# Optimization experiments

Measured on AMD Instinct MI355X. Metric: run time of the kernel, lower is better.

## Reference

```python
import jax, jax.numpy as jnp
import numpy as np

B, C, L = 8, 512, 8192
H = 8  # head_count
DK = C // H  # head key channels
DV = C // H  # head value channels


def setup_inputs() -> dict:
    key = jax.random.key(0)
    ks = jax.random.split(key, 10)
    s = 1.0 / np.sqrt(C)
    return {
        "input_": jax.random.normal(ks[0], (B, C, L), jnp.float32),
        "context_": jax.random.normal(ks[1], (B, C, L), jnp.float32),
        "Wk": jax.random.normal(ks[2], (C, C), jnp.float32) * s,
        "bk": jax.random.normal(ks[3], (C,), jnp.float32) * 0.01,
        "Wq": jax.random.normal(ks[4], (C, C), jnp.float32) * s,
        "bq": jax.random.normal(ks[5], (C,), jnp.float32) * 0.01,
        "Wv": jax.random.normal(ks[6], (C, C), jnp.float32) * s,
        "bv": jax.random.normal(ks[7], (C,), jnp.float32) * 0.01,
        "Wr": jax.random.normal(ks[8], (C, C), jnp.float32) * s,
        "br": jax.random.normal(ks[9], (C,), jnp.float32) * 0.01,
    }


def _proj(W, b, x):
    # 1x1 Conv1d == channel matmul: [O,C] x [B,C,L] -> [B,O,L]
    return jnp.einsum('oc,bcl->bol', W, x) + b[None, :, None]


def reference(input_, context_, Wk, bk, Wq, bq, Wv, bv, Wr, br):
    b, _, l = input_.shape
    keys = _proj(Wk, bk, context_).reshape(b, H, DK, l)
    queries = _proj(Wq, bq, input_).reshape(b, H, DK, l)
    values = _proj(Wv, bv, context_).reshape(b, H, DV, l)
    # per-head: softmax(K) over sequence, softmax(Q) over head-key channels
    k = jax.nn.softmax(keys, axis=3)
    q = jax.nn.softmax(queries, axis=2)
    # context = K @ V^T : [b,h,dk,dv]
    ctx = jnp.einsum('bhkl,bhvl->bhkv', k, values)
    # attended = context^T @ Q : [b,h,dv,l]
    att = jnp.einsum('bhkv,bhkl->bhvl', ctx, q).reshape(b, H * DV, l)
    return _proj(Wr, br, att) + input_
```

## Files before the change

kernel.cpp:

```cpp
#include <hip/hip_runtime.h>

#define NB 8
#define NC 512
#define NL 8192
#define NH 8
#define ND 64

typedef float f32x4 __attribute__((ext_vector_type(4)));
typedef __bf16 bf16x8 __attribute__((ext_vector_type(8)));
typedef unsigned int u32x4 __attribute__((ext_vector_type(4)));

__device__ __forceinline__ unsigned short f2bf(float f) {
    unsigned u = __builtin_bit_cast(unsigned, f);
    u += 0x7fffu + ((u >> 16) & 1u);
    return (unsigned short)(u >> 16);
}
__device__ __forceinline__ bf16x8 frag_from_u32x4(u32x4 v) {
    return __builtin_bit_cast(bf16x8, v);
}
__device__ __forceinline__ bf16x8 ld_frag_lds(const unsigned short* p) {
    const unsigned* q = (const unsigned*)p;
    u32x4 v = { q[0], q[1], q[2], q[3] };
    return frag_from_u32x4(v);
}
__device__ __forceinline__ bf16x8 ld_frag_g16(const unsigned short* p) {
    return frag_from_u32x4(*(const u32x4*)p);
}
__device__ __forceinline__ bf16x8 ldL(const unsigned short* Lb, unsigned off) {
    return frag_from_u32x4(*(const u32x4*)((const char*)Lb + off));
}

__device__ __forceinline__ void gload16(const unsigned short* g, unsigned short* l) {
    __builtin_amdgcn_global_load_lds(
        (const __attribute__((address_space(1))) unsigned int*)g,
        (__attribute__((address_space(3))) unsigned int*)l, 16, 0, 0);
}

__device__ __forceinline__ void prep_body(int i,
    const float* __restrict__ Wk, const float* __restrict__ Wv,
    const float* __restrict__ Wq, const float* __restrict__ Wr,
    const float* __restrict__ bk, const float* __restrict__ bv,
    unsigned short* __restrict__ Wb, float* __restrict__ bkv, float* __restrict__ zf)
{
    const int WN = NC * NC;
    if (i < 4 * WN) {
        const float* src = (i < WN) ? Wk : (i < 2 * WN) ? Wv : (i < 3 * WN) ? Wq : Wr;
        Wb[i] = f2bf(src[i & (WN - 1)]);
    } else if (i < 4 * WN + 2 * NC) {
        int j = i - 4 * WN;
        bkv[j] = (j < NC) ? bk[j] : bv[j - NC];
    } else {
        zf[i - (4 * WN + 2 * NC)] = 0.f;
    }
}

__device__ __forceinline__ int ltidx(int c, int l) {
    return c * 64 + ((((l) >> 2) ^ ((c >> 2) & 15)) << 2) + (l & 3);
}
__global__ __launch_bounds__(256) void transpose_prep_kernel(
    const float* __restrict__ X0, const float* __restrict__ X1,
    unsigned short* __restrict__ Y0, unsigned short* __restrict__ Y1,
    const float* __restrict__ Wk, const float* __restrict__ Wv,
    const float* __restrict__ Wq, const float* __restrict__ Wr,
    const float* __restrict__ bk, const float* __restrict__ bv,
    unsigned short* __restrict__ Wb, float* __restrict__ bkv, float* __restrict__ zf)
{
    const int bz = blockIdx.z;
    const int t = threadIdx.x;
    if (bz == 2 * NB) {
        constexpr int total = 4 * NC * NC + 2 * NC + (NB * NH * ND * ND + NB * NC);
        const int stride = (NL / 64) * (NC / 64) * 256;
        for (int i = (blockIdx.y * (NL / 64) + blockIdx.x) * 256 + t; i < total; i += stride)
            prep_body(i, Wk, Wv, Wq, Wr, bk, bv, Wb, bkv, zf);
        return;
    }
    const float* X = (bz < NB) ? X0 : X1;
    unsigned short* Y = (bz < NB) ? Y0 : Y1;
    const int b = bz & (NB - 1);
    const int l0 = blockIdx.x * 64, c0 = blockIdx.y * 64;
    __shared__ alignas(16) unsigned short lt[64 * 64];
    const float* Xb = X + (size_t)b * NC * NL;
    #pragma unroll
    for (int it = 0; it < 4; ++it) {
        const int c = it * 16 + (t >> 4), l4 = (t & 15) * 4;
        f32x4 v = *(const f32x4*)(Xb + (size_t)(c0 + c) * NL + l0 + l4);
        unsigned lo = f2bf(v.x) | ((unsigned)f2bf(v.y) << 16);
        unsigned hi = f2bf(v.z) | ((unsigned)f2bf(v.w) << 16);
        unsigned* p = (unsigned*)&lt[ltidx(c, l4)];
        p[0] = lo; p[1] = hi;
    }
    __syncthreads();
    unsigned short* Yb = Y + (size_t)b * NL * NC;
    #pragma unroll
    for (int it = 0; it < 2; ++it) {
        const int l = it * 32 + (t >> 3), c8 = (t & 7) * 8;
        u32x4 o;
        #pragma unroll
        for (int d = 0; d < 4; ++d) {
            unsigned lo = lt[ltidx(c8 + 2 * d, l)];
            unsigned hi = lt[ltidx(c8 + 2 * d + 1, l)];
            o[d] = lo | (hi << 16);
        }
        *(u32x4*)(Yb + (size_t)(l0 + l) * NC + c0 + c8) = o;
    }
}

__device__ __forceinline__ void stage_half(
    unsigned short* __restrict__ Ld, const unsigned short* __restrict__ Gs,
    int t, int wave)
{
    #pragma unroll
    for (int c = 0; c < 2; ++c) {
        const int idx = c * 512 + t;
        const int r = idx >> 3;
        const int ch = (idx & 7) ^ (r & 7);
        gload16(Gs + (size_t)r * NC + ch * 8, Ld + (size_t)(c * 512 + wave * 64) * 8);
    }
}

template<int MT, bool RESID, bool PERB, bool EXPK>
__global__ __launch_bounds__(512) void gemm8_kernel(
    const unsigned short* __restrict__ Wb,
    const unsigned short* __restrict__ Xt,
    const float* __restrict__ bias,
    const float* __restrict__ resid,
    void* __restrict__ Yv)
{
    const int bx = blockIdx.x;
    const int g  = bx >> 3;
    const int mt = g % MT;
    const int nt = (g / MT) * 8 + (bx & 7);
    const int b  = blockIdx.y;
    const int t  = threadIdx.x;
    const int wave = t >> 6, lane = t & 63;
    const int m0 = mt * 256, n0 = nt * 256;
    const int wm = wave >> 2, wn = wave & 3;
    const int OC = MT * 256;

    __shared__ alignas(16) unsigned short L[65536];

    f32x4 acc[8][4] = {};

    const unsigned short* Wp = Wb + (PERB ? (size_t)b * NC * NC : 0) + (size_t)m0 * NC;
    const unsigned short* Xp = Xt + (size_t)b * NL * NC + (size_t)n0 * NC;

    const int lr = lane & 15, qg = lane >> 4;
    const unsigned xr = (unsigned)(lr & 7);
    const unsigned cq0 = (((unsigned)qg) ^ xr) * 16u;
    const unsigned cq1 = (((unsigned)qg + 4u) ^ xr) * 16u;
    const unsigned aB = (unsigned)(wm * 16384 + lr * 128);
    const unsigned bB = 32768u + (unsigned)((wn >> 1) * 16384 + ((wn & 1) * 64 + lr) * 128);

    #define STA(par, half, kt) stage_half(&L[(par) * 32768 + (half) * 8192], \
        Wp + (size_t)((half) * 128) * NC + (kt) * 64, t, wave)
    #define STB(par, half, kt) stage_half(&L[(par) * 32768 + 16384 + (half) * 8192], \
        Xp + (size_t)((half) * 128) * NC + (kt) * 64, t, wave)

    STA(0, 0, 0); STA(0, 1, 0); STB(0, 0, 0); STB(0, 1, 0);
    STA(1, 0, 1); STA(1, 1, 1); STB(1, 0, 1); STB(1, 1, 1);
    __builtin_amdgcn_sched_barrier(0);
    asm volatile("s_waitcnt vmcnt(8)" ::: "memory");
    __builtin_amdgcn_sched_barrier(0);
    __builtin_amdgcn_s_barrier();
    __builtin_amdgcn_sched_barrier(0);

    for (int kt = 0; kt < 8; ++kt) {
        const unsigned parB = (unsigned)((kt & 1) * 65536);
        const int par = kt & 1, ks = kt + 2;
        bf16x8 bf[4][2];
        #pragma unroll
        for (int q4 = 0; q4 < 4; ++q4) {
            if (q4 == 0) {
                #pragma unroll
                for (int j = 0; j < 4; ++j) {
                    bf[j][0] = ldL(L, parB + bB + j * 2048 + cq0);
                    bf[j][1] = ldL(L, parB + bB + j * 2048 + cq1);
                }
            }
            bf16x8 af[2][2];
            #pragma unroll
            for (int di = 0; di < 2; ++di) {
                af[di][0] = ldL(L, parB + aB + (q4 * 2 + di) * 2048 + cq0);
                af[di][1] = ldL(L, parB + aB + (q4 * 2 + di) * 2048 + cq1);
            }
            if (ks < 8) {
                if (q4 == 1)      { STB(par, 0, ks); }
                else if (q4 == 2) { STB(par, 1, ks); }
                else if (q4 == 3) { STA(par, 0, ks); STA(par, 1, ks); }
            }
            __builtin_amdgcn_sched_barrier(0);
            __builtin_amdgcn_s_barrier();
            __builtin_amdgcn_sched_barrier(0);
            __builtin_amdgcn_s_setprio(1);
            #pragma unroll
            for (int di = 0; di < 2; ++di)
                #pragma unroll
                for (int j = 0; j < 4; ++j) {
                    acc[q4 * 2 + di][j] = __builtin_amdgcn_mfma_f32_16x16x32_bf16(
                        af[di][0], bf[j][0], acc[q4 * 2 + di][j], 0, 0, 0);
                    acc[q4 * 2 + di][j] = __builtin_amdgcn_mfma_f32_16x16x32_bf16(
                        af[di][1], bf[j][1], acc[q4 * 2 + di][j], 0, 0, 0);
                }
            __builtin_amdgcn_s_setprio(0);
            __builtin_amdgcn_sched_barrier(0);
            if (q4 == 3) {
                if (kt < 6)       asm volatile("s_waitcnt vmcnt(8)" ::: "memory");
                else if (kt == 6) asm volatile("s_waitcnt vmcnt(0)" ::: "memory");
                __builtin_amdgcn_sched_barrier(0);
            }
            __builtin_amdgcn_s_barrier();
            __builtin_amdgcn_sched_barrier(0);
        }
    }
    #undef STA
    #undef STB

    const int col = lr, row0 = qg * 4;
    if constexpr (EXPK) {
        unsigned short* Y = (unsigned short*)Yv;
        const bool isK = (m0 < NC);
        #pragma unroll
        for (int i = 0; i < 8; ++i)
            #pragma unroll
            for (int r = 0; r < 4; ++r) {
                const int o = m0 + wm * 128 + i * 16 + row0 + r;
                const float bo = bias[o];
                const size_t rb = (size_t)b * OC * NL + (size_t)o * NL + n0 + wn * 64;
                #pragma unroll
                for (int j = 0; j < 4; ++j) {
                    float v = acc[i][j][r] + bo;
                    if (isK) v = __expf(v);
                    Y[rb + j * 16 + col] = f2bf(v);
                }
            }
    } else if constexpr (RESID) {
        float* Y = (float*)Yv;
        #pragma unroll
        for (int i = 0; i < 8; ++i)
            #pragma unroll
            for (int r = 0; r < 4; ++r) {
                const int o = m0 + wm * 128 + i * 16 + row0 + r;
                const float bo = bias[o];
                const size_t rb = (size_t)b * OC * NL + (size_t)o * NL + n0 + wn * 64;
                #pragma unroll
                for (int j = 0; j < 4; ++j) {
                    const size_t idx = rb + j * 16 + col;
                    Y[idx] = acc[i][j][r] + bo + resid[idx];
                }
            }
    } else {
        unsigned short* Y = (unsigned short*)Yv;
        #pragma unroll
        for (int i = 0; i < 8; ++i)
            #pragma unroll
            for (int r = 0; r < 4; ++r) {
                const int o = m0 + wm * 128 + i * 16 + row0 + r;
                const float bo = bias[o];
                const size_t rb = (size_t)b * OC * NL + (size_t)o * NL + n0 + wn * 64;
                #pragma unroll
                for (int j = 0; j < 4; ++j)
                    Y[rb + j * 16 + col] = f2bf(acc[i][j][r] + bo);
            }
    }
}

template<int MT, bool RESID, bool PERB, bool QSMT, bool EXPK>
__global__ __launch_bounds__(256) void gemm_kernel(
    const unsigned short* __restrict__ Wb,
    const unsigned short* __restrict__ Xt,
    const float* __restrict__ bias,
    const float* __restrict__ resid,
    void* __restrict__ Yv)
{
    const int bx = blockIdx.x;
    const int g  = bx >> 3;
    const int mt = g % MT;
    const int nt = (g / MT) * 8 + (bx & 7);
    const int b  = blockIdx.y;
    const int t  = threadIdx.x;
    const int wave = t >> 6, lane = t & 63;
    const int m0 = mt * 128, n0 = nt * 128;
    const int wm = (wave & 1) * 64, wn = (wave >> 1) * 64;
    const int OC = MT * 128;

    __shared__ alignas(16) unsigned short lA[128 * 32];
    __shared__ alignas(16) unsigned short lX[128 * 32];

    f32x4 acc[4][4] = {};

    const unsigned short* Wp = Wb + (PERB ? (size_t)b * NC * NC : 0);
    const unsigned short* Xb = Xt + (size_t)b * NL * NC;

    const int lr = lane & 15, q = lane >> 4;
    const unsigned aoff = (unsigned)((wm + lr) * 64 + (q ^ (((wm + lr) >> 1) & 3)) * 16);
    const unsigned boff = (unsigned)((wn + lr) * 64 + (q ^ (((wn + lr) >> 1) & 3)) * 16);
    const int pb0 = wave * 128;

    for (int k0 = 0; k0 < NC; k0 += 32) {
        #pragma unroll
        for (int cc = 0; cc < 2; ++cc) {
            const int pb = pb0 + cc * 64;
            const int p  = pb + lane;
            const int r  = p >> 2;
            const int qq = (p & 3) ^ ((r >> 1) & 3);
            gload16(Wp + (size_t)(m0 + r) * NC + k0 + qq * 8, &lA[pb * 8]);
            gload16(Xb + (size_t)(n0 + r) * NC + k0 + qq * 8, &lX[pb * 8]);
        }
        __syncthreads();

        bf16x8 af[4], bfx[4];
        #pragma unroll
        for (int i = 0; i < 4; ++i)
            af[i] = frag_from_u32x4(*(const u32x4*)((const char*)lA + aoff + i * 1024));
        #pragma unroll
        for (int j = 0; j < 4; ++j)
            bfx[j] = frag_from_u32x4(*(const u32x4*)((const char*)lX + boff + j * 1024));
        #pragma unroll
        for (int i = 0; i < 4; ++i)
            #pragma unroll
            for (int j = 0; j < 4; ++j)
                acc[i][j] = __builtin_amdgcn_mfma_f32_16x16x32_bf16(af[i], bfx[j], acc[i][j], 0, 0, 0);
        __syncthreads();
    }

    const int col = lane & 15, row0 = (lane >> 4) * 4;

    if constexpr (QSMT) {
        #pragma unroll
        for (int i = 0; i < 4; ++i)
            #pragma unroll
            for (int r = 0; r < 4; ++r) {
                const float bo = bias[m0 + wm + i * 16 + row0 + r];
                #pragma unroll
                for (int j = 0; j < 4; ++j) acc[i][j][r] += bo;
            }
        float inv[4];
        #pragma unroll
        for (int j = 0; j < 4; ++j) {
            float m = -1e30f;
            #pragma unroll
            for (int i = 0; i < 4; ++i)
                #pragma unroll
                for (int r = 0; r < 4; ++r) m = fmaxf(m, acc[i][j][r]);
            m = fmaxf(m, __shfl_xor(m, 16));
            m = fmaxf(m, __shfl_xor(m, 32));
            float s = 0.f;
            #pragma unroll
            for (int i = 0; i < 4; ++i)
                #pragma unroll
                for (int r = 0; r < 4; ++r) {
                    const float e = __expf(acc[i][j][r] - m);
                    acc[i][j][r] = e;
                    s += e;
                }
            s += __shfl_xor(s, 16);
            s += __shfl_xor(s, 32);
            inv[j] = 1.0f / s;
        }
        unsigned short* Yq = (unsigned short*)Yv;
        #pragma unroll
        for (int j = 0; j < 4; ++j) {
            const size_t rowb = (size_t)b * NL * NC + (size_t)(n0 + wn + j * 16 + col) * NC;
            #pragma unroll
            for (int i = 0; i < 4; ++i) {
                const int o0 = m0 + wm + i * 16 + row0;
                unsigned lo = f2bf(acc[i][j][0] * inv[j]) | ((unsigned)f2bf(acc[i][j][1] * inv[j]) << 16);
                unsigned hi = f2bf(acc[i][j][2] * inv[j]) | ((unsigned)f2bf(acc[i][j][3] * inv[j]) << 16);
                *(unsigned long long*)(Yq + rowb + o0) =
                    (unsigned long long)lo | ((unsigned long long)hi << 32);
            }
        }
    } else if constexpr (EXPK) {
        unsigned short* Y = (unsigned short*)Yv;
        const bool isK = (m0 < NC);
        #pragma unroll
        for (int i = 0; i < 4; ++i)
            #pragma unroll
            for (int r = 0; r < 4; ++r) {
                const int o = m0 + wm + i * 16 + row0 + r;
                const float bo = bias[o];
                const size_t rb = (size_t)b * OC * NL + (size_t)o * NL + n0 + wn;
                #pragma unroll
                for (int j = 0; j < 4; ++j) {
                    float v = acc[i][j][r] + bo;
                    if (isK) v = __expf(v);
                    Y[rb + j * 16 + col] = f2bf(v);
                }
            }
    } else {
        #pragma unroll
        for (int i = 0; i < 4; ++i) {
            #pragma unroll
            for (int r = 0; r < 4; ++r) {
                const int o = m0 + wm + i * 16 + row0 + r;
                const float bo = bias[o];
                const size_t rb = (size_t)b * OC * NL + (size_t)o * NL + n0 + wn;
                if constexpr (RESID) {
                    float* Y = (float*)Yv;
                    #pragma unroll
                    for (int j = 0; j < 4; ++j) {
                        const size_t idx = rb + j * 16 + col;
                        Y[idx] = acc[i][j][r] + bo + resid[idx];
                    }
                } else {
                    unsigned short* Y = (unsigned short*)Yv;
                    #pragma unroll
                    for (int j = 0; j < 4; ++j)
                        Y[rb + j * 16 + col] = f2bf(acc[i][j][r] + bo);
                }
            }
        }
    }
}

__global__ __launch_bounds__(256) void ctx_kernel(
    const unsigned short* __restrict__ KV,
    float* __restrict__ ctx,
    float* __restrict__ rowsum)
{
    const int bh = blockIdx.x;
    const int sp = blockIdx.y;
    const int t = threadIdx.x;
    const int wave = t >> 6, lane = t & 63;
    const int b = bh >> 3, h = bh & 7;
    const size_t base_k = ((size_t)b * 2 * NC + h * ND) * NL;
    const size_t base_v = base_k + (size_t)NC * NL;
    const int i = wave * 16 + (lane & 15);
    const int koff = (lane >> 4) * 8;
    const unsigned short* Ka = KV + base_k + (size_t)i * NL + koff;

    const u32x4 onesw = { 0x3f803f80u, 0x3f803f80u, 0x3f803f80u, 0x3f803f80u };
    const bf16x8 onef = frag_from_u32x4(onesw);

    f32x4 acc[4] = {};
    f32x4 accs = {};
    const int l0 = sp * (NL / 16);
    for (int l = l0; l < l0 + (NL / 16); l += 32) {
        bf16x8 a = ld_frag_g16(Ka + l);
        #pragma unroll
        for (int j = 0; j < 4; ++j) {
            bf16x8 bv = ld_frag_g16(KV + base_v + (size_t)(j * 16 + (lane & 15)) * NL + l + koff);
            acc[j] = __builtin_amdgcn_mfma_f32_16x16x32_bf16(a, bv, acc[j], 0, 0, 0);
        }
        accs = __builtin_amdgcn_mfma_f32_16x16x32_bf16(a, onef, accs, 0, 0, 0);
    }
    const int col = lane & 15, row0 = (lane >> 4) * 4;
    #pragma unroll
    for (int j = 0; j < 4; ++j)
        #pragma unroll
        for (int r = 0; r < 4; ++r)
            atomicAdd(&ctx[(size_t)bh * (ND * ND) + (size_t)(wave * 16 + row0 + r) * ND + j * 16 + col],
                      acc[j][r]);
    if (col == 0) {
        #pragma unroll
        for (int r = 0; r < 4; ++r)
            atomicAdd(&rowsum[(size_t)b * NC + h * ND + wave * 16 + row0 + r], accs[r]);
    }
}

__global__ __launch_bounds__(512) void fold_kernel(
    const unsigned short* __restrict__ Wrb,
    const float* __restrict__ ctxb,
    const float* __restrict__ rowsum,
    unsigned short* __restrict__ Mb)
{
    const int bh = blockIdx.x;
    const int b = bh >> 3, h = bh & 7;
    const int t = threadIdx.x;
    const int wave = t >> 6, lane = t & 63;

    __shared__ unsigned short lc[64 * 66];
    const float* cs = ctxb + (size_t)bh * (ND * ND);
    const float* rs = rowsum + (size_t)b * NC + h * ND;
    #pragma unroll
    for (int it = 0; it < 8; ++it) {
        int i = it * 512 + t;
        lc[(i >> 6) * 66 + (i & 63)] = f2bf(cs[i] / rs[i >> 6]);
    }
    __syncthreads();

    const int koff = (lane >> 4) * 8;
    f32x4 acc[4][4] = {};
    #pragma unroll
    for (int kk = 0; kk < 64; kk += 32) {
        bf16x8 af[4], bfx[4];
        #pragma unroll
        for (int i = 0; i < 4; ++i)
            af[i] = ld_frag_g16(Wrb + (size_t)(wave * 64 + i * 16 + (lane & 15)) * NC
                                + h * ND + kk + koff);
        #pragma unroll
        for (int j = 0; j < 4; ++j)
            bfx[j] = ld_frag_lds(&lc[(j * 16 + (lane & 15)) * 66 + kk + koff]);
        #pragma unroll
        for (int i = 0; i < 4; ++i)
            #pragma unroll
            for (int j = 0; j < 4; ++j)
                acc[i][j] = __builtin_amdgcn_mfma_f32_16x16x32_bf16(af[i], bfx[j], acc[i][j], 0, 0, 0);
    }

    const int col = lane & 15, row0 = (lane >> 4) * 4;
    #pragma unroll
    for (int i = 0; i < 4; ++i)
        #pragma unroll
        for (int r = 0; r < 4; ++r) {
            const int o = wave * 64 + i * 16 + row0 + r;
            #pragma unroll
            for (int j = 0; j < 4; ++j)
                Mb[(size_t)b * NC * NC + (size_t)o * NC + h * ND + j * 16 + col]
                    = f2bf(acc[i][j][r]);
        }
}

extern "C" void kernel_launch(void* const* d_in, const int* in_sizes, int n_in,
                              void* d_out, int out_size, void* d_ws, size_t ws_size,
                              hipStream_t stream) {
    (void)in_sizes; (void)n_in; (void)out_size; (void)ws_size;
    const float* input_   = (const float*)d_in[0];
    const float* context_ = (const float*)d_in[1];
    const float* Wk = (const float*)d_in[2];
    const float* bk = (const float*)d_in[3];
    const float* Wq = (const float*)d_in[4];
    const float* bq = (const float*)d_in[5];
    const float* Wv = (const float*)d_in[6];
    const float* bv = (const float*)d_in[7];
    const float* Wr = (const float*)d_in[8];
    const float* br = (const float*)d_in[9];
    float* out = (float*)d_out;

    char* ws = (char*)d_ws;
    unsigned short* Wkvb = (unsigned short*)ws;
    unsigned short* Wqb  = Wkvb + 2 * NC * NC;
    unsigned short* Wrb  = Wqb + NC * NC;
    float* bkv  = (float*)(Wrb + NC * NC);
    float* ctxb = bkv + 2 * NC;
    float* rowsum = ctxb + NB * NH * ND * ND;
    unsigned short* KVp = (unsigned short*)(rowsum + NB * NC);
    unsigned short* R2  = KVp + (size_t)NB * 2 * NC * NL;
    unsigned short* Mb  = KVp;
    unsigned short* Xt_in = (unsigned short*)d_out;

    transpose_prep_kernel<<<dim3(NL / 64, NC / 64, 2 * NB + 1), 256, 0, stream>>>(
        context_, input_, R2, Xt_in,
        Wk, Wv, Wq, Wr, bk, bv, Wkvb, bkv, ctxb);

    gemm8_kernel<4, false, false, true><<<dim3(128, NB), 512, 0, stream>>>(
        Wkvb, R2, bkv, nullptr, KVp);

    gemm_kernel<4, false, false, true, false><<<dim3(256, NB), 256, 0, stream>>>(
        Wqb, Xt_in, bq, nullptr, R2);

    ctx_kernel<<<dim3(NB * NH, 16), 256, 0, stream>>>(KVp, ctxb, rowsum);
    fold_kernel<<<NB * NH, 512, 0, stream>>>(Wrb, ctxb, rowsum, Mb);

    gemm8_kernel<2, true, true, false><<<dim3(64, NB), 512, 0, stream>>>(
        Mb, R2, br, input_, out);
}
```

Measured before the change: 621.8 us.

## Move Q projection with softmax epilogue onto 256x256 gemm8 kernel; widen transpose tiles

Removes the older 128x128 gemm_kernel. The Q projection and its fused per-head channel softmax now run on the pipelined 512-thread gemm8 kernel with 256x256 tiles, where each wave covers two heads. This targets better data reuse and MFMA pipelining for the Q GEMM. The input transpose kernel also now handles 256 channels per block instead of 64, cutting the block count and using a larger LDS tile. In exchange, the grids are smaller, which risks lower occupancy and a heavier register load in the softmax epilogue.

```diff
diff --git a/kernel.cpp b/kernel.cpp
--- a/kernel.cpp
+++ b/kernel.cpp
@@ -69,7 +69,7 @@
     const int t = threadIdx.x;
     if (bz == 2 * NB) {
         constexpr int total = 4 * NC * NC + 2 * NC + (NB * NH * ND * ND + NB * NC);
-        const int stride = (NL / 64) * (NC / 64) * 256;
+        const int stride = (NL / 64) * (NC / 256) * 256;
         for (int i = (blockIdx.y * (NL / 64) + blockIdx.x) * 256 + t; i < total; i += stride)
             prep_body(i, Wk, Wv, Wq, Wr, bk, bv, Wb, bkv, zf);
         return;
@@ -77,11 +77,11 @@
     const float* X = (bz < NB) ? X0 : X1;
     unsigned short* Y = (bz < NB) ? Y0 : Y1;
     const int b = bz & (NB - 1);
-    const int l0 = blockIdx.x * 64, c0 = blockIdx.y * 64;
-    __shared__ alignas(16) unsigned short lt[64 * 64];
+    const int l0 = blockIdx.x * 64, c0 = blockIdx.y * 256;
+    __shared__ alignas(16) unsigned short lt[256 * 64];
     const float* Xb = X + (size_t)b * NC * NL;
     #pragma unroll
-    for (int it = 0; it < 4; ++it) {
+    for (int it = 0; it < 16; ++it) {
         const int c = it * 16 + (t >> 4), l4 = (t & 15) * 4;
         f32x4 v = *(const f32x4*)(Xb + (size_t)(c0 + c) * NL + l0 + l4);
         unsigned lo = f2bf(v.x) | ((unsigned)f2bf(v.y) << 16);
@@ -92,8 +92,8 @@
     __syncthreads();
     unsigned short* Yb = Y + (size_t)b * NL * NC;
     #pragma unroll
-    for (int it = 0; it < 2; ++it) {
-        const int l = it * 32 + (t >> 3), c8 = (t & 7) * 8;
+    for (int it = 0; it < 8; ++it) {
+        const int l = it * 8 + (t >> 5), c8 = (t & 31) * 8;
         u32x4 o;
         #pragma unroll
         for (int d = 0; d < 4; ++d) {
@@ -118,7 +118,7 @@
     }
 }
 
-template<int MT, bool RESID, bool PERB, bool EXPK>
+template<int MT, bool RESID, bool PERB, bool EXPK, bool QSMT>
 __global__ __launch_bounds__(512) void gemm8_kernel(
     const unsigned short* __restrict__ Wb,
     const unsigned short* __restrict__ Xt,
@@ -216,7 +216,55 @@
     #undef STB
 
     const int col = lr, row0 = qg * 4;
-    if constexpr (EXPK) {
+    if constexpr (QSMT) {
+        #pragma unroll
+        for (int i = 0; i < 8; ++i)
+            #pragma unroll
+            for (int r = 0; r < 4; ++r) {
+                const float bo = bias[m0 + wm * 128 + i * 16 + row0 + r];
+                #pragma unroll
+                for (int j = 0; j < 4; ++j) acc[i][j][r] += bo;
+            }
+        float inv[2][4];
+        #pragma unroll
+        for (int hh = 0; hh < 2; ++hh)
+            #pragma unroll
+            for (int j = 0; j < 4; ++j) {
+                float m = -1e30f;
+                #pragma unroll
+                for (int i = 0; i < 4; ++i)
+                    #pragma unroll
+                    for (int r = 0; r < 4; ++r) m = fmaxf(m, acc[hh * 4 + i][j][r]);
+                m = fmaxf(m, __shfl_xor(m, 16));
+                m = fmaxf(m, __shfl_xor(m, 32));
+                float s = 0.f;
+                #pragma unroll
+                for (int i = 0; i < 4; ++i)
+                    #pragma unroll
+                    for (int r = 0; r < 4; ++r) {
+                        const float e = __expf(acc[hh * 4 + i][j][r] - m);
+                        acc[hh * 4 + i][j][r] = e;
+                        s += e;
+                    }
+                s += __shfl_xor(s, 16);
+                s += __shfl_xor(s, 32);
+                inv[hh][j] = 1.0f / s;
+            }
+        unsigned short* Yq = (unsigned short*)Yv;
+        #pragma unroll
+        for (int j = 0; j < 4; ++j) {
+            const size_t rowb = (size_t)b * NL * NC + (size_t)(n0 + wn * 64 + j * 16 + col) * NC;
+            #pragma unroll
+            for (int i = 0; i < 8; ++i) {
+                const float iv = inv[i >> 2][j];
+                const int o0 = m0 + wm * 128 + i * 16 + row0;
+                unsigned lo = f2bf(acc[i][j][0] * iv) | ((unsigned)f2bf(acc[i][j][1] * iv) << 16);
+                unsigned hi = f2bf(acc[i][j][2] * iv) | ((unsigned)f2bf(acc[i][j][3] * iv) << 16);
+                *(unsigned long long*)(Yq + rowb + o0) =
+                    (unsigned long long)lo | ((unsigned long long)hi << 32);
+            }
+        }
+    } else if constexpr (EXPK) {
         unsigned short* Y = (unsigned short*)Yv;
         const bool isK = (m0 < NC);
         #pragma unroll
@@ -261,155 +309,6 @@
                 for (int j = 0; j < 4; ++j)
                     Y[rb + j * 16 + col] = f2bf(acc[i][j][r] + bo);
             }
-    }
-}
-
-template<int MT, bool RESID, bool PERB, bool QSMT, bool EXPK>
-__global__ __launch_bounds__(256) void gemm_kernel(
-    const unsigned short* __restrict__ Wb,
-    const unsigned short* __restrict__ Xt,
-    const float* __restrict__ bias,
-    const float* __restrict__ resid,
-    void* __restrict__ Yv)
-{
-    const int bx = blockIdx.x;
-    const int g  = bx >> 3;
-    const int mt = g % MT;
-    const int nt = (g / MT) * 8 + (bx & 7);
-    const int b  = blockIdx.y;
-    const int t  = threadIdx.x;
-    const int wave = t >> 6, lane = t & 63;
-    const int m0 = mt * 128, n0 = nt * 128;
-    const int wm = (wave & 1) * 64, wn = (wave >> 1) * 64;
-    const int OC = MT * 128;
-
-    __shared__ alignas(16) unsigned short lA[128 * 32];
-    __shared__ alignas(16) unsigned short lX[128 * 32];
-
-    f32x4 acc[4][4] = {};
-
-    const unsigned short* Wp = Wb + (PERB ? (size_t)b * NC * NC : 0);
-    const unsigned short* Xb = Xt + (size_t)b * NL * NC;
-
-    const int lr = lane & 15, q = lane >> 4;
-    const unsigned aoff = (unsigned)((wm + lr) * 64 + (q ^ (((wm + lr) >> 1) & 3)) * 16);
-    const unsigned boff = (unsigned)((wn + lr) * 64 + (q ^ (((wn + lr) >> 1) & 3)) * 16);
-    const int pb0 = wave * 128;
-
-    for (int k0 = 0; k0 < NC; k0 += 32) {
-        #pragma unroll
-        for (int cc = 0; cc < 2; ++cc) {
-            const int pb = pb0 + cc * 64;
-            const int p  = pb + lane;
-            const int r  = p >> 2;
-            const int qq = (p & 3) ^ ((r >> 1) & 3);
-            gload16(Wp + (size_t)(m0 + r) * NC + k0 + qq * 8, &lA[pb * 8]);
-            gload16(Xb + (size_t)(n0 + r) * NC + k0 + qq * 8, &lX[pb * 8]);
-        }
-        __syncthreads();
-
-        bf16x8 af[4], bfx[4];
-        #pragma unroll
-        for (int i = 0; i < 4; ++i)
-            af[i] = frag_from_u32x4(*(const u32x4*)((const char*)lA + aoff + i * 1024));
-        #pragma unroll
-        for (int j = 0; j < 4; ++j)
-            bfx[j] = frag_from_u32x4(*(const u32x4*)((const char*)lX + boff + j * 1024));
-        #pragma unroll
-        for (int i = 0; i < 4; ++i)
-            #pragma unroll
-            for (int j = 0; j < 4; ++j)
-                acc[i][j] = __builtin_amdgcn_mfma_f32_16x16x32_bf16(af[i], bfx[j], acc[i][j], 0, 0, 0);
-        __syncthreads();
-    }
-
-    const int col = lane & 15, row0 = (lane >> 4) * 4;
-
-    if constexpr (QSMT) {
-        #pragma unroll
-        for (int i = 0; i < 4; ++i)
-            #pragma unroll
-            for (int r = 0; r < 4; ++r) {
-                const float bo = bias[m0 + wm + i * 16 + row0 + r];
-                #pragma unroll
-                for (int j = 0; j < 4; ++j) acc[i][j][r] += bo;
-            }
-        float inv[4];
-        #pragma unroll
-        for (int j = 0; j < 4; ++j) {
-            float m = -1e30f;
-            #pragma unroll
-            for (int i = 0; i < 4; ++i)
-                #pragma unroll
-                for (int r = 0; r < 4; ++r) m = fmaxf(m, acc[i][j][r]);
-            m = fmaxf(m, __shfl_xor(m, 16));
-            m = fmaxf(m, __shfl_xor(m, 32));
-            float s = 0.f;
-            #pragma unroll
-            for (int i = 0; i < 4; ++i)
-                #pragma unroll
-                for (int r = 0; r < 4; ++r) {
-                    const float e = __expf(acc[i][j][r] - m);
-                    acc[i][j][r] = e;
-                    s += e;
-                }
-            s += __shfl_xor(s, 16);
-            s += __shfl_xor(s, 32);
-            inv[j] = 1.0f / s;
-        }
-        unsigned short* Yq = (unsigned short*)Yv;
-        #pragma unroll
-        for (int j = 0; j < 4; ++j) {
-            const size_t rowb = (size_t)b * NL * NC + (size_t)(n0 + wn + j * 16 + col) * NC;
-            #pragma unroll
-            for (int i = 0; i < 4; ++i) {
-                const int o0 = m0 + wm + i * 16 + row0;
-                unsigned lo = f2bf(acc[i][j][0] * inv[j]) | ((unsigned)f2bf(acc[i][j][1] * inv[j]) << 16);
-                unsigned hi = f2bf(acc[i][j][2] * inv[j]) | ((unsigned)f2bf(acc[i][j][3] * inv[j]) << 16);
-                *(unsigned long long*)(Yq + rowb + o0) =
-                    (unsigned long long)lo | ((unsigned long long)hi << 32);
-            }
-        }
-    } else if constexpr (EXPK) {
-        unsigned short* Y = (unsigned short*)Yv;
-        const bool isK = (m0 < NC);
-        #pragma unroll
-        for (int i = 0; i < 4; ++i)
-            #pragma unroll
-            for (int r = 0; r < 4; ++r) {
-                const int o = m0 + wm + i * 16 + row0 + r;
-                const float bo = bias[o];
-                const size_t rb = (size_t)b * OC * NL + (size_t)o * NL + n0 + wn;
-                #pragma unroll
-                for (int j = 0; j < 4; ++j) {
-                    float v = acc[i][j][r] + bo;
-                    if (isK) v = __expf(v);
-                    Y[rb + j * 16 + col] = f2bf(v);
-                }
-            }
-    } else {
-        #pragma unroll
-        for (int i = 0; i < 4; ++i) {
-            #pragma unroll
-            for (int r = 0; r < 4; ++r) {
-                const int o = m0 + wm + i * 16 + row0 + r;
-                const float bo = bias[o];
-                const size_t rb = (size_t)b * OC * NL + (size_t)o * NL + n0 + wn;
-                if constexpr (RESID) {
-                    float* Y = (float*)Yv;
-                    #pragma unroll
-                    for (int j = 0; j < 4; ++j) {
-                        const size_t idx = rb + j * 16 + col;
-                        Y[idx] = acc[i][j][r] + bo + resid[idx];
-                    }
-                } else {
-                    unsigned short* Y = (unsigned short*)Yv;
-                    #pragma unroll
-                    for (int j = 0; j < 4; ++j)
-                        Y[rb + j * 16 + col] = f2bf(acc[i][j][r] + bo);
-                }
-            }
-        }
     }
 }
 
@@ -539,19 +438,19 @@
     unsigned short* Mb  = KVp;
     unsigned short* Xt_in = (unsigned short*)d_out;
 
-    transpose_prep_kernel<<<dim3(NL / 64, NC / 64, 2 * NB + 1), 256, 0, stream>>>(
+    transpose_prep_kernel<<<dim3(NL / 64, NC / 256, 2 * NB + 1), 256, 0, stream>>>(
         context_, input_, R2, Xt_in,
         Wk, Wv, Wq, Wr, bk, bv, Wkvb, bkv, ctxb);
 
-    gemm8_kernel<4, false, false, true><<<dim3(128, NB), 512, 0, stream>>>(
+    gemm8_kernel<4, false, false, true, false><<<dim3(128, NB), 512, 0, stream>>>(
         Wkvb, R2, bkv, nullptr, KVp);
 
-    gemm_kernel<4, false, false, true, false><<<dim3(256, NB), 256, 0, stream>>>(
+    gemm8_kernel<2, false, false, false, true><<<dim3(64, NB), 512, 0, stream>>>(
         Wqb, Xt_in, bq, nullptr, R2);
 
     ctx_kernel<<<dim3(NB * NH, 16), 256, 0, stream>>>(KVp, ctxb, rowsum);
     fold_kernel<<<NB * NH, 512, 0, stream>>>(Wrb, ctxb, rowsum, Mb);
 
-    gemm8_kernel<2, true, true, false><<<dim3(64, NB), 512, 0, stream>>>(
+    gemm8_kernel<2, true, true, false, false><<<dim3(64, NB), 512, 0, stream>>>(
         Mb, R2, br, input_, out);
 }
```

Result: no change. 618.8 us (-0.5%).
